# Kernel optimization log

Measured on AMD Instinct MI355X. Metric: run time of the kernel, lower is better.

## Reference

```python
import jax, jax.numpy as jnp
import numpy as np

N_HEADS = 16
ROPE_THETA = 10000.0


def _rope(x):
    # x: (b, h, t, d). Interleaved-pair rotary embedding (lucidrains
    # rotary_embedding_torch convention: rotate_half on (d r) pairs, r=2).
    b, h, t, d = x.shape
    inv_freq = 1.0 / (ROPE_THETA ** (jnp.arange(0, d, 2, dtype=jnp.float32) / d))  # (d/2,)
    ang = jnp.arange(t, dtype=jnp.float32)[:, None] * inv_freq[None, :]            # (t, d/2)
    cos = jnp.cos(ang)
    sin = jnp.sin(ang)
    xp = x.reshape(b, h, t, d // 2, 2)
    x1, x2 = xp[..., 0], xp[..., 1]
    o1 = x1 * cos - x2 * sin
    o2 = x1 * sin + x2 * cos
    return jnp.stack([o1, o2], axis=-1).reshape(b, h, t, d)


def setup_inputs() -> dict:
    key = jax.random.key(0)
    k1, k2, k3 = jax.random.split(key, 3)
    B, T, C = 4, 2048, 1024
    x = jax.random.normal(k1, (B, T, C), dtype=jnp.float32)
    # torch nn.Linear weight layout: (out_features, in_features)
    w_attn = jax.random.normal(k2, (3 * C, C), dtype=jnp.float32) * (1.0 / np.sqrt(C))
    w_proj = jax.random.normal(k3, (C, C), dtype=jnp.float32) * (1.0 / np.sqrt(C))
    return {"x": x, "w_attn": w_attn, "w_proj": w_proj}


def reference(x, w_attn, w_proj):
    B, T, C = x.shape
    H = N_HEADS
    D = C // H
    # fused QKV projection: (b, t, 3C)
    qkv = jnp.einsum('btc,fc->btf', x, w_attn)
    # rearrange 'b t (r h d) -> r b h t d'
    qkv = qkv.reshape(B, T, 3, H, D).transpose(2, 0, 3, 1, 4)
    q, k, v = qkv[0], qkv[1], qkv[2]
    q = _rope(q)
    k = _rope(k)
    scale = 1.0 / np.sqrt(D).astype(np.float32)
    scores = jnp.einsum('bhqd,bhkd->bhqk', q, k) * scale
    attn = jax.nn.softmax(scores, axis=-1)
    y = jnp.einsum('bhqk,bhkd->bhqd', attn, v)       # (b, h, t, d)
    y = y.transpose(0, 2, 1, 3).reshape(B, T, C)     # 'b h t d -> b t (h d)'
    return jnp.einsum('btc,oc->bto', y, w_proj)
```

## Files before the change

kernel.cpp:

```cpp
#include <hip/hip_runtime.h>
#include <hip/hip_bf16.h>
#include <math.h>

typedef __bf16 bf16;
typedef float f32x4 __attribute__((ext_vector_type(4)));
typedef float f32x16 __attribute__((ext_vector_type(16)));
typedef bf16 bf16x8 __attribute__((ext_vector_type(8)));
typedef bf16 bf16x4 __attribute__((ext_vector_type(4)));
typedef unsigned int uint;
typedef uint uintx2 __attribute__((ext_vector_type(2)));

#define MFMA16(a, b, c) __builtin_amdgcn_mfma_f32_16x16x32_bf16(a, b, c, 0, 0, 0)
#define MFMA32(a, b, c) __builtin_amdgcn_mfma_f32_32x32x16_bf16(a, b, c, 0, 0, 0)

static constexpr int T_SEQ = 2048;
static constexpr int CDIM  = 1024;
static constexpr int NH    = 16;
static constexpr int DH    = 64;
static constexpr float FREQ_C = 0.20762050593045998f;
static constexpr float Q_SCALE = 0.18033688011112042f;

__device__ __forceinline__ float fexp2(float x) {
    return __builtin_amdgcn_exp2f(x);
}

__device__ __forceinline__ uint pack_bf16(float lo, float hi) {
    union { bf16 h[2]; uint u; } cv;
    cv.h[0] = (bf16)lo;
    cv.h[1] = (bf16)hi;
    return cv.u;
}

__device__ __forceinline__ void gld_lds16(const bf16* g, bf16* l) {
    __builtin_amdgcn_global_load_lds(
        (const __attribute__((address_space(1))) void*)g,
        (__attribute__((address_space(3))) void*)l, 16, 0, 0);
}

__device__ __forceinline__ void fast_sincos(float x, float* s, float* c) {
    const float INV2PI = 0.15915494309189535f;
    const float PI2_HI = 6.28125f;
    const float PI2_LO = 1.9353071795864769e-3f;
    const float n = rintf(x * INV2PI);
    float r = fmaf(-n, PI2_HI, x);
    r = fmaf(-n, PI2_LO, r);
    *s = __sinf(r);
    *c = __cosf(r);
}

__global__ __launch_bounds__(256)
void rope_table(float2* __restrict__ tab) {
    const int i = blockIdx.x * 256 + threadIdx.x;
    const int t = i >> 5, p = i & 31;
    const float ang = (float)t * exp2f(-2.0f * (float)p * FREQ_C);
    float s, c;
    fast_sincos(ang, &s, &c);
    tab[i] = make_float2(c, s);
}

__global__ __launch_bounds__(256)
void cvt_f32_bf16(const float* __restrict__ in, bf16* __restrict__ out, int n8) {
    const int i = blockIdx.x * 256 + threadIdx.x;
    if (i >= n8) return;
    const f32x4* p = (const f32x4*)(in + (size_t)i * 8);
    const f32x4 lo = p[0], hi = p[1];
    bf16x8 o;
    o[0] = (bf16)lo[0]; o[1] = (bf16)lo[1]; o[2] = (bf16)lo[2]; o[3] = (bf16)lo[3];
    o[4] = (bf16)hi[0]; o[5] = (bf16)hi[1]; o[6] = (bf16)hi[2]; o[7] = (bf16)hi[3];
    *(bf16x8*)(out + (size_t)i * 8) = o;
}

#define GEMM_STAGE(buf_, kk_, Abase, Bbase, KDIM) do {                           \
        _Pragma("unroll")                                                        \
        for (int u = 0; u < 4; u++) {                                            \
            const int st = wave * 4 + u, mg = st >> 1, kg = st & 1;              \
            gld_lds16((Abase) + (size_t)(mg * 16 + sm) * (KDIM) + (kk_) + kg * 32 + sc * 8, \
                      &ash[buf_][st * 512]);                                     \
            gld_lds16((Bbase) + (size_t)(mg * 16 + sm) * (KDIM) + (kk_) + kg * 32 + sc * 8, \
                      &bsh[buf_][st * 512]);                                     \
        }                                                                        \
    } while (0)

#define GEMM_CORE(Abase, Bbase, KDIM)                                            \
    f32x4 acc[4][4] = {};                                                        \
    GEMM_STAGE(0, 0, Abase, Bbase, KDIM);                                        \
    int ibuf = 0;                                                                \
    for (int kk = 0; kk < (KDIM); kk += 64, ibuf ^= 1) {                         \
        __syncthreads();       \
        if (kk + 64 < (KDIM))                                                    \
            GEMM_STAGE(ibuf ^ 1, kk + 64, Abase, Bbase, KDIM);                   \
        _Pragma("unroll")                                                        \
        for (int kg = 0; kg < 2; kg++) {                                         \
            bf16x8 af[4], bfr[4];                                                \
            _Pragma("unroll")                                                    \
            for (int a = 0; a < 4; a++)                                          \
                af[a] = *(const bf16x8*)&ash[ibuf][((wm * 4 + a) * 2 + kg) * 512 + lane * 8]; \
            _Pragma("unroll")                                                    \
            for (int b = 0; b < 4; b++)                                          \
                bfr[b] = *(const bf16x8*)&bsh[ibuf][((wn * 4 + b) * 2 + kg) * 512 + lane * 8]; \
            _Pragma("unroll")                                                    \
            for (int a = 0; a < 4; a++)                                          \
                _Pragma("unroll")                                                \
                for (int b = 0; b < 4; b++)                                      \
                    acc[a][b] = MFMA16(af[a], bfr[b], acc[a][b]);                \
        }                                                                        \
    }

__global__ __launch_bounds__(256)
void gemm_qkv(const bf16* __restrict__ X, const bf16* __restrict__ W,
              bf16* __restrict__ Qo, bf16* __restrict__ Ko, bf16* __restrict__ Vt,
              const float2* __restrict__ tab) {
    __shared__ __align__(16) bf16 ash[2][16 * 512];
    __shared__ __align__(16) bf16 bsh[2][16 * 512];
    const int tid = threadIdx.x, lane = tid & 63, wave = tid >> 6;
    const int quad = lane >> 4, l16 = lane & 15;
    const int wm = wave >> 1, wn = wave & 1;
    const int bm = blockIdx.y, bn = blockIdx.x;
    const int sm = lane & 15, sc = lane >> 4;

    const bf16* Abase = X + (size_t)(bm * 128) * CDIM;
    const bf16* Bbase = W + (size_t)(bn * 128) * CDIM;
    GEMM_CORE(Abase, Bbase, CDIM)

    const int rr    = (bn * 128) >> 10;
    const int nsec  = (bn * 128) & 1023;
    const int batch = (bm * 128) >> 11;
    const int tb    = ((bm * 128) & 2047) + wm * 64;

    if (rr == 2) {
#pragma unroll
        for (int b = 0; b < 4; b++) {
            const int n = nsec + wn * 64 + b * 16 + l16;
            const int h = n >> 6, d = n & 63;
            bf16* vp = Vt + ((size_t)(batch * NH + h) * DH + d) * T_SEQ;
#pragma unroll
            for (int a = 0; a < 4; a++) {
                const int t0 = tb + a * 16 + quad * 4;
                bf16x4 pk4 = { (bf16)acc[a][b][0], (bf16)acc[a][b][1],
                               (bf16)acc[a][b][2], (bf16)acc[a][b][3] };
                *(bf16x4*)(vp + t0) = pk4;
            }
        }
    } else {
        bf16* Dst = (rr == 0) ? Qo : Ko;
        const float scale = (rr == 0) ? Q_SCALE : 1.0f;
#pragma unroll
        for (int b = 0; b < 4; b++) {
            const int n = nsec + wn * 64 + b * 16 + l16;
            const int h = n >> 6, d = n & 63;
            const int p = d >> 1, odd = d & 1;
            bf16* dp = Dst + (size_t)(batch * NH + h) * T_SEQ * DH + d;
#pragma unroll
            for (int a = 0; a < 4; a++) {
#pragma unroll
                for (int r = 0; r < 4; r++) {
                    const int t = tb + a * 16 + quad * 4 + r;
                    const float val = acc[a][b][r];
                    const float partner = __shfl_xor(val, 1);
                    const float2 cs = tab[t * 32 + p];
                    float o = odd ? (partner * cs.y + val * cs.x)
                                  : (val * cs.x - partner * cs.y);
                    dp[(size_t)t * DH] = (bf16)(o * scale);
                }
            }
        }
    }
}

__global__ __launch_bounds__(256)
void gemm_proj(const bf16* __restrict__ X, const bf16* __restrict__ W,
               float* __restrict__ Out) {
    __shared__ __align__(16) bf16 ash[2][16 * 512];
    __shared__ __align__(16) bf16 bsh[2][16 * 512];
    const int tid = threadIdx.x, lane = tid & 63, wave = tid >> 6;
    const int quad = lane >> 4, l16 = lane & 15;
    const int wm = wave >> 1, wn = wave & 1;
    const int bm = blockIdx.y, bn = blockIdx.x;
    const int sm = lane & 15, sc = lane >> 4;

    const bf16* Abase = X + (size_t)(bm * 128) * CDIM;
    const bf16* Bbase = W + (size_t)(bn * 128) * CDIM;
    GEMM_CORE(Abase, Bbase, CDIM)

#pragma unroll
    for (int b = 0; b < 4; b++) {
        const int n = bn * 128 + wn * 64 + b * 16 + l16;
#pragma unroll
        for (int a = 0; a < 4; a++) {
            const int m = bm * 128 + wm * 64 + a * 16 + quad * 4;
#pragma unroll
            for (int r = 0; r < 4; r++)
                Out[(size_t)(m + r) * CDIM + n] = acc[a][b][r];
        }
    }
}

__global__ __launch_bounds__(256)
void flash(const bf16* __restrict__ Q, const bf16* __restrict__ K,
           const bf16* __restrict__ Vt, bf16* __restrict__ Y) {
    __shared__ __align__(16) bf16 ksh[2][8 * 512];
    __shared__ __align__(16) bf16 vsh[2][8 * 512];
    const int tid = threadIdx.x, lane = tid & 63, wave = tid >> 6;
    const int l32 = lane & 31, hi = lane >> 5;
    const int id = blockIdx.x;
    const int bh = (id & 7) * 8 + ((id >> 3) & 7);
    const int qsb = id >> 6;
    const size_t kbase = (size_t)bh * T_SEQ * DH;
    const size_t vbase = (size_t)bh * DH * T_SEQ;
    const int q0 = qsb * 256 + wave * 32;

    bf16x8 bq[2][4];
#pragma unroll
    for (int tq = 0; tq < 2; tq++) {
        const bf16* qp = Q + kbase + (size_t)(q0 + tq * 128 + l32) * DH + hi * 8;
#pragma unroll
        for (int c = 0; c < 4; c++) bq[tq][c] = *(const bf16x8*)(qp + c * 16);
    }

    f32x16 oT[2][2] = {};
    f32x16 lf[2] = {};
    bf16x8 onesf;
#pragma unroll
    for (int j = 0; j < 8; j++) onesf[j] = (bf16)1.0f;

#define STAGE(buf_, kt_) do {                                              \
        if (wave < 2) {                                                    \
            _Pragma("unroll")                                              \
            for (int u = 0; u < 4; u++) {                                  \
                const int s = wave * 4 + u, kb = s >> 2, c = s & 3;        \
                gld_lds16(K + kbase + (size_t)((kt_) + kb * 32 + l32) * DH \
                              + c * 16 + hi * 8,                           \
                          &ksh[buf_][s * 512]);                            \
            }                                                              \
        } else {                                                           \
            _Pragma("unroll")                                              \
            for (int u = 0; u < 4; u++) {                                  \
                const int s = (wave - 2) * 4 + u, db = s >> 2, kc = s & 3; \
                gld_lds16(Vt + vbase + (size_t)(db * 32 + l32) * T_SEQ     \
                              + (kt_) + kc * 16 + hi * 8,                  \
                          &vsh[buf_][s * 512]);                            \
            }                                                              \
        }                                                                  \
    } while (0)

    STAGE(0, 0);
    int ib = 0;
    for (int kt = 0; kt < T_SEQ; kt += 64, ib ^= 1) {
        __syncthreads();
        if (kt + 64 < T_SEQ) STAGE(ib ^ 1, kt + 64);

#pragma unroll
        for (int kb = 0; kb < 2; kb++) {
            f32x16 s0 = {}, s1 = {};
#pragma unroll
            for (int c = 0; c < 4; c++) {
                const bf16x8 a = *(const bf16x8*)&ksh[ib][(kb * 4 + c) * 512 + lane * 8];
                s0 = MFMA32(a, bq[0][c], s0);
                s1 = MFMA32(a, bq[1][c], s1);
            }
            uint P[2][8];
#pragma unroll
            for (int w = 0; w < 8; w++) {
                P[0][w] = pack_bf16(fexp2(s0[2 * w]), fexp2(s0[2 * w + 1]));
                P[1][w] = pack_bf16(fexp2(s1[2 * w]), fexp2(s1[2 * w + 1]));
            }
#pragma unroll
            for (int t = 0; t < 2; t++) {
                const int kc = kb * 2 + t;
                bf16x8 vv[2];
#pragma unroll
                for (int db = 0; db < 2; db++)
                    vv[db] = *(const bf16x8*)&vsh[ib][(db * 4 + kc) * 512 + lane * 8];
#pragma unroll
                for (int tq = 0; tq < 2; tq++) {
                    const uintx2 rA = __builtin_amdgcn_permlane32_swap(
                        P[tq][4 * t + 0], P[tq][4 * t + 2], false, false);
                    const uintx2 rB = __builtin_amdgcn_permlane32_swap(
                        P[tq][4 * t + 1], P[tq][4 * t + 3], false, false);
                    union { uint u[4]; bf16x8 v; } bP;
                    bP.u[0] = rA[0]; bP.u[1] = rB[0];
                    bP.u[2] = rA[1]; bP.u[3] = rB[1];
                    lf[tq] = MFMA32(onesf, bP.v, lf[tq]);
#pragma unroll
                    for (int db = 0; db < 2; db++)
                        oT[tq][db] = MFMA32(vv[db], bP.v, oT[tq][db]);
                }
            }
        }
    }
#undef STAGE

    const int b = bh >> 4, h = bh & 15;
#pragma unroll
    for (int tq = 0; tq < 2; tq++) {
        const float inv = 1.0f / lf[tq][0];
        const size_t yrow =
            ((size_t)b * T_SEQ + q0 + tq * 128 + l32) * CDIM + h * DH;
#pragma unroll
        for (int db = 0; db < 2; db++)
#pragma unroll
            for (int rg = 0; rg < 4; rg++) {
                bf16x4 o4 = { (bf16)(oT[tq][db][rg * 4 + 0] * inv),
                              (bf16)(oT[tq][db][rg * 4 + 1] * inv),
                              (bf16)(oT[tq][db][rg * 4 + 2] * inv),
                              (bf16)(oT[tq][db][rg * 4 + 3] * inv) };
                *(bf16x4*)(Y + yrow + db * 32 + 8 * rg + 4 * hi) = o4;
            }
    }
}

extern "C" void kernel_launch(void* const* d_in, const int* in_sizes, int n_in,
                              void* d_out, int out_size, void* d_ws, size_t ws_size,
                              hipStream_t stream) {
    const float* x      = (const float*)d_in[0];
    const float* w_attn = (const float*)d_in[1];
    const float* w_proj = (const float*)d_in[2];
    float* out = (float*)d_out;

    bf16* ws = (bf16*)d_ws;
    const size_t SZ = (size_t)4 * NH * T_SEQ * DH;
    bf16* Xb  = ws;
    bf16* Wab = Xb + SZ;
    bf16* Wpb = Wab + 3145728;
    bf16* Qb  = Wpb + 1048576;
    bf16* Kb  = Qb + SZ;
    bf16* Vtb = Kb + SZ;
    bf16* Yb  = Vtb + SZ;
    float2* tab = (float2*)(Yb + SZ);

    rope_table<<<256, 256, 0, stream>>>(tab);
    cvt_f32_bf16<<<4096, 256, 0, stream>>>(x, Xb, 1048576);
    cvt_f32_bf16<<<1536, 256, 0, stream>>>(w_attn, Wab, 393216);
    cvt_f32_bf16<<<512, 256, 0, stream>>>(w_proj, Wpb, 131072);

    gemm_qkv<<<dim3(24, 64), 256, 0, stream>>>(Xb, Wab, Qb, Kb, Vtb, tab);
    flash<<<512, 256, 0, stream>>>(Qb, Kb, Vtb, Yb);
    gemm_proj<<<dim3(8, 64), 256, 0, stream>>>(Yb, Wpb, out);
}
```

Measured before the change: 346.5 us.

## Pipeline GEMM loads with explicit vmcnt waits and XCD-aware block swizzle

The GEMM main loop now issues the next stage's global-to-LDS loads first and waits only for the previous stage with s_waitcnt vmcnt(8). Raw s_barrier and sched_barrier calls replace __syncthreads so that in-flight prefetches overlap the MFMA work. Both GEMM kernels also remap block indices so that each XCD gets a contiguous group of row tiles sharing A rows, to improve L2 locality. The hand-placed waitcnt counts depend on how many loads each stage issues and could become wrong if the compiler changes its load emission.

New measurement: 328.2 us. -5.3%, faster.

```diff
diff --git a/kernel.cpp b/kernel.cpp
--- a/kernel.cpp
+++ b/kernel.cpp
@@ -74,36 +74,43 @@
         _Pragma("unroll")                                                        \
         for (int u = 0; u < 4; u++) {                                            \
             const int st = wave * 4 + u, mg = st >> 1, kg = st & 1;              \
-            gld_lds16((Abase) + (size_t)(mg * 16 + sm) * (KDIM) + (kk_) + kg * 32 + sc * 8, \
-                      &ash[buf_][st * 512]);                                     \
-            gld_lds16((Bbase) + (size_t)(mg * 16 + sm) * (KDIM) + (kk_) + kg * 32 + sc * 8, \
-                      &bsh[buf_][st * 512]);                                     \
+            const size_t off = (size_t)(mg * 16 + sm) * (KDIM) + (kk_)           \
+                               + kg * 32 + sc * 8;                               \
+            gld_lds16((Abase) + off, &ash[buf_][st * 512]);                      \
+            gld_lds16((Bbase) + off, &bsh[buf_][st * 512]);                      \
         }                                                                        \
     } while (0)
 
 #define GEMM_CORE(Abase, Bbase, KDIM)                                            \
     f32x4 acc[4][4] = {};                                                        \
     GEMM_STAGE(0, 0, Abase, Bbase, KDIM);                                        \
-    int ibuf = 0;                                                                \
-    for (int kk = 0; kk < (KDIM); kk += 64, ibuf ^= 1) {                         \
-        __syncthreads();       \
-        if (kk + 64 < (KDIM))                                                    \
-            GEMM_STAGE(ibuf ^ 1, kk + 64, Abase, Bbase, KDIM);                   \
+    for (int kk = 0; kk < (KDIM); kk += 64) {                                    \
+        const int cur = (kk >> 6) & 1;                                           \
+        if (kk + 64 < (KDIM)) {                                                  \
+            GEMM_STAGE(cur ^ 1, kk + 64, Abase, Bbase, KDIM);                    \
+            __builtin_amdgcn_sched_barrier(0);                                   \
+            asm volatile("s_waitcnt vmcnt(8)" ::: "memory");                     \
+        } else {                                                                 \
+            asm volatile("s_waitcnt vmcnt(0)" ::: "memory");                     \
+        }                                                                        \
+        __builtin_amdgcn_s_barrier();                                            \
+        __builtin_amdgcn_sched_barrier(0);                                       \
         _Pragma("unroll")                                                        \
         for (int kg = 0; kg < 2; kg++) {                                         \
             bf16x8 af[4], bfr[4];                                                \
             _Pragma("unroll")                                                    \
-            for (int a = 0; a < 4; a++)                                          \
-                af[a] = *(const bf16x8*)&ash[ibuf][((wm * 4 + a) * 2 + kg) * 512 + lane * 8]; \
-            _Pragma("unroll")                                                    \
-            for (int b = 0; b < 4; b++)                                          \
-                bfr[b] = *(const bf16x8*)&bsh[ibuf][((wn * 4 + b) * 2 + kg) * 512 + lane * 8]; \
+            for (int a = 0; a < 4; a++) {                                        \
+                af[a]  = *(const bf16x8*)&ash[cur][((wm * 4 + a) * 2 + kg) * 512 + lane * 8]; \
+                bfr[a] = *(const bf16x8*)&bsh[cur][((wn * 4 + a) * 2 + kg) * 512 + lane * 8]; \
+            }                                                                    \
             _Pragma("unroll")                                                    \
             for (int a = 0; a < 4; a++)                                          \
                 _Pragma("unroll")                                                \
                 for (int b = 0; b < 4; b++)                                      \
                     acc[a][b] = MFMA16(af[a], bfr[b], acc[a][b]);                \
         }                                                                        \
+        __builtin_amdgcn_sched_barrier(0);                                       \
+        __builtin_amdgcn_s_barrier();                                            \
     }
 
 __global__ __launch_bounds__(256)
@@ -115,7 +122,9 @@
     const int tid = threadIdx.x, lane = tid & 63, wave = tid >> 6;
     const int quad = lane >> 4, l16 = lane & 15;
     const int wm = wave >> 1, wn = wave & 1;
-    const int bm = blockIdx.y, bn = blockIdx.x;
+    const int lin = blockIdx.y * 24 + blockIdx.x;
+    const int xcd = lin & 7, j = lin >> 3;
+    const int bm = xcd * 8 + (j & 7), bn = j >> 3;
     const int sm = lane & 15, sc = lane >> 4;
 
     const bf16* Abase = X + (size_t)(bm * 128) * CDIM;
@@ -175,7 +184,9 @@
     const int tid = threadIdx.x, lane = tid & 63, wave = tid >> 6;
     const int quad = lane >> 4, l16 = lane & 15;
     const int wm = wave >> 1, wn = wave & 1;
-    const int bm = blockIdx.y, bn = blockIdx.x;
+    const int lin = blockIdx.y * 8 + blockIdx.x;
+    const int xcd = lin & 7, j = lin >> 3;
+    const int bm = xcd * 8 + (j & 7), bn = j >> 3;
     const int sm = lane & 15, sc = lane >> 4;
 
     const bf16* Abase = X + (size_t)(bm * 128) * CDIM;
```
